# Kernel tuning notes

Measured on AMD Instinct MI355X. Metric: run time of the kernel, lower is better.

## Reference

```python
import jax, jax.numpy as jnp
import numpy as np

EPS = 1e-5


def _layernorm(x, w, b):
    mu = jnp.mean(x, axis=-1, keepdims=True)
    var = jnp.mean(jnp.square(x - mu), axis=-1, keepdims=True)
    return (x - mu) * jax.lax.rsqrt(var + EPS) * w + b


def setup_inputs() -> dict:
    key = jax.random.key(0)
    ks = jax.random.split(key, 8)
    B, N, D = 1, 512, 128
    x = jax.random.normal(ks[0], (B, N, N, D), dtype=jnp.float32)
    mask = jnp.round(jax.random.uniform(ks[1], (B, N, N), dtype=jnp.float32) * 0.6 + 0.4)
    # LayerNorm params (input_norm: ones/zeros; output_norm: ones/zeros)
    ln1_w = jnp.ones((D,), jnp.float32)
    ln1_b = jnp.zeros((D,), jnp.float32)
    ln2_w = jnp.ones((D // 2,), jnp.float32)
    ln2_b = jnp.zeros((D // 2,), jnp.float32)
    # Linear weights stored (in, out). pi: lecun-normal; gi/go: gating init (zeros w, ones b); po: final init (zeros) -> use small randn for a nontrivial baseline.
    sd = 1.0 / np.sqrt(D)
    pi_w = jax.random.normal(ks[2], (D, D), jnp.float32) * sd
    pi_b = jnp.zeros((D,), jnp.float32)
    gi_w = jax.random.normal(ks[3], (D, D), jnp.float32) * sd
    gi_b = jnp.ones((D,), jnp.float32)
    sd2 = 1.0 / np.sqrt(D // 2)
    po_w = jax.random.normal(ks[4], (D // 2, D), jnp.float32) * sd2
    po_b = jnp.zeros((D,), jnp.float32)
    go_w = jax.random.normal(ks[5], (D // 2, D), jnp.float32) * sd2
    go_b = jnp.ones((D,), jnp.float32)
    return {"x": x, "mask": mask, "ln1_w": ln1_w, "ln1_b": ln1_b,
            "pi_w": pi_w, "pi_b": pi_b, "gi_w": gi_w, "gi_b": gi_b,
            "ln2_w": ln2_w, "ln2_b": ln2_b, "po_w": po_w, "po_b": po_b,
            "go_w": go_w, "go_b": go_b}


def reference(x, mask, ln1_w, ln1_b, pi_w, pi_b, gi_w, gi_b,
              ln2_w, ln2_b, po_w, po_b, go_w, go_b):
    # project_and_gate: LN -> pi/gi linears -> sigmoid gate -> mask
    h = _layernorm(x, ln1_w, ln1_b)                      # (B,N,N,D)
    pi_out = h @ pi_w + pi_b
    gi_logits = h @ gi_w + gi_b
    g = pi_out * jax.nn.sigmoid(gi_logits) * mask[..., None]
    # triangular multiplication: split channels into 4 groups of D/4
    a1, b1, a2, b2 = jnp.split(g, 4, axis=-1)            # each (B,N,N,D/4)
    x1 = jnp.einsum('bikd,bjkd->bijd', a1, b1)           # k_dim=2 (outgoing)
    x2 = jnp.einsum('bkid,bkjd->bijd', a2, b2)           # k_dim=1 (incoming)
    t = jnp.concatenate([x1, x2], axis=-1)               # (B,N,N,D/2)
    # output: LN -> po/go linears -> sigmoid gate -> mask
    t = _layernorm(t, ln2_w, ln2_b)
    po_out = t @ po_w + po_b                             # (B,N,N,D)
    go_logits = t @ go_w + go_b
    return po_out * jax.nn.sigmoid(go_logits) * mask[..., None]
```

## Files before the change

kernel.cpp:

```cpp
#include <hip/hip_runtime.h>
#include <hip/hip_bf16.h>

#define NDIM 512
#define NN   (NDIM * NDIM)


using short8 = __attribute__((ext_vector_type(8))) short;
using f32x4  = __attribute__((ext_vector_type(4))) float;
typedef unsigned int uint32;
typedef unsigned short ushort;

__device__ __forceinline__ float sigmoidf_(float z) { return 1.f / (1.f + __expf(-z)); }
__device__ __forceinline__ uint32 pkbf2(float a, float b) {
    __hip_bfloat162 h = __float22bfloat162_rn(float2{a, b});
    uint32 u; __builtin_memcpy(&u, &h, 4); return u;
}
__device__ __forceinline__ ushort bfbits(float f) {
    __hip_bfloat16 h = __float2bfloat16(f);
    ushort u; __builtin_memcpy(&u, &h, 2); return u;
}
__device__ __forceinline__ float bf2f(ushort h) {
    return __uint_as_float(((uint32)h) << 16);
}

__global__ void k_prep(const float* __restrict__ Wp, const float* __restrict__ Wg,
                       const float* __restrict__ lnw, const float* __restrict__ lnb,
                       const float* __restrict__ bp, const float* __restrict__ bg,
                       int K, ushort* __restrict__ dst, float* __restrict__ cb)
{
    __shared__ float red[2][2][128];
    const int nbp = (K * 128) / 256;
    const int tid = threadIdx.x;
    if ((int)blockIdx.x < nbp) {
        const int idx = blockIdx.x * 256 + tid;
        const int k = idx >> 7, o = idx & 127;
        int rowp, rowg;
        if (K == 128) {
            const int h = o >> 6, c = o & 63, q = c >> 5, s = c & 31;
            rowp = h * 128 + q * 64 + s;
            rowg = rowp + 32;
        } else {
            const int q = o >> 6, s = o & 63;
            rowp = q * 128 + s;
            rowg = rowp + 64;
        }
        const float wk = lnw[k];
        const float vp = Wp[k * 128 + o] * wk;
        const float vg = Wg[k * 128 + o] * wk;
        ushort hi;
        hi = bfbits(vp);
        dst[rowp * K + k] = hi;
        dst[256 * K + rowp * K + k] = bfbits(vp - bf2f(hi));
        hi = bfbits(vg);
        dst[rowg * K + k] = hi;
        dst[256 * K + rowg * K + k] = bfbits(vg - bf2f(hi));
    } else {
        const int b = blockIdx.x - nbp;
        const float* W = b ? Wg : Wp;
        const float* bias = b ? bg : bp;
        const int o = tid & 127, kh = tid >> 7;
        const int kham = K >> 1;
        const int k0 = kh * kham;
        float c1 = 0.f, c2 = 0.f;
#pragma unroll 8
        for (int k = 0; k < kham; ++k) {
            const float wv = W[(k0 + k) * 128 + o];
            c1 = fmaf(lnw[k0 + k], wv, c1);
            c2 = fmaf(lnb[k0 + k], wv, c2);
        }
        red[kh][0][o] = c1; red[kh][1][o] = c2;
        __syncthreads();
        if (kh == 0) {
            const int base = b ? 256 : 0;
            cb[base + o] = red[0][0][o] + red[1][0][o];
            cb[base + 128 + o] = red[0][1][o] + red[1][1][o] + bias[o];
        }
    }
}

__global__ __launch_bounds__(256, 4)
void k_stage1(const float* __restrict__ x, const float* __restrict__ mask,
              const ushort* __restrict__ wt1, const float* __restrict__ cb,
              ushort* __restrict__ wsg)
{
    __shared__ char sbuf[32768];
    __shared__ float Ms[128], Mu[128], Rs[128];

    const int tid = threadIdx.x;
    const int g  = blockIdx.x;
    const int y  = (g >> 3) & 1;
    const int bx = (g & 7) | ((g >> 4) << 3);
    const int o0 = y * 64;
    const int w = tid >> 6, l = tid & 63;
    const int mrow = (w & 1) * 64, ncol = (w >> 1) * 64;

    long posBase, outBase; int stride;
    if (y == 0) {
        posBase = ((long)(bx >> 2)) * 512 + (long)(bx & 3) * 128;
        outBase = posBase; stride = 1;
    } else {
        posBase = ((long)(bx >> 9)) * 65536 + (bx & 511);
        outBase = (long)(bx & 511) * 512 + ((bx >> 9) * 128);
        stride = 512;
    }

    short8 bh[2][4], bl[2][4];
#pragma unroll
    for (int n = 0; n < 4; ++n) {
        const int row = y*128 + ncol + n*16 + (l & 15);
        const int idx = row*128 + (l >> 4)*8;
        bh[0][n] = *(const short8*)(wt1 + idx);
        bl[0][n] = *(const short8*)(wt1 + 32768 + idx);
    }

    {
#pragma unroll
        for (int q = 0; q < 16; ++q) {
            const int idx = q*256 + tid;
            const int pos = idx >> 5, fg = idx & 31;
            const float4 v = *(const float4*)(x + (posBase + (long)pos*stride)*128 + fg*4);
            uint2 pk;
            pk.x = pkbf2(v.x, v.y);
            pk.y = pkbf2(v.z, v.w);
            const int col = (fg*8) ^ ((pos & 15) << 4);
            *(uint2*)(sbuf + pos*256 + col) = pk;
        }
        if (tid < 128) Ms[tid] = mask[posBase + (long)tid * stride];
    }
    __syncthreads();

    {
        const int r = tid >> 1, hf = tid & 1;
        float s = 0.f, ss = 0.f;
#pragma unroll
        for (int c = 0; c < 8; ++c) {
            const int col = (hf*128 + c*16) ^ ((r & 15) << 4);
            const short8 hv = *(const short8*)(sbuf + r*256 + col);
#pragma unroll
            for (int e = 0; e < 8; ++e) {
                const float tv = bf2f((ushort)hv[e]);
                s += tv; ss = fmaf(tv, tv, ss);
            }
        }
        s  += __shfl_xor(s, 1);
        ss += __shfl_xor(ss, 1);
        const float mu = s * (1.f/128.f);
        const float var = ss * (1.f/128.f) - mu*mu;
        const float rstd = rsqrtf(var + 1e-5f);
        if (hf == 0) { Mu[r] = mu; Rs[r] = rstd; }
    }

    f32x4 acc[4][4];
#pragma unroll
    for (int m = 0; m < 4; ++m)
#pragma unroll
        for (int n = 0; n < 4; ++n) acc[m][n] = (f32x4){0.f,0.f,0.f,0.f};

#pragma unroll
    for (int step = 0; step < 4; ++step) {
        if (step < 3) {
            const int s1 = step + 1;
#pragma unroll
            for (int n = 0; n < 4; ++n) {
                const int row = y*128 + ncol + n*16 + (l & 15);
                const int idx = row*128 + s1*32 + (l >> 4)*8;
                bh[s1 & 1][n] = *(const short8*)(wt1 + idx);
                bl[s1 & 1][n] = *(const short8*)(wt1 + 32768 + idx);
            }
        }
        short8 ah[4];
#pragma unroll
        for (int m = 0; m < 4; ++m) {
            const int pos = mrow + m*16 + (l & 15);
            const int col = (step*64 + (l >> 4)*16) ^ ((pos & 15) << 4);
            ah[m] = *(const short8*)(sbuf + pos*256 + col);
        }
#pragma unroll
        for (int m = 0; m < 4; ++m) {
#pragma unroll
            for (int n = 0; n < 4; ++n) {
                acc[m][n] = __builtin_amdgcn_mfma_f32_16x16x32_bf16(ah[m], bh[step & 1][n], acc[m][n], 0, 0, 0);
                acc[m][n] = __builtin_amdgcn_mfma_f32_16x16x32_bf16(ah[m], bl[step & 1][n], acc[m][n], 0, 0, 0);
            }
        }
    }
    __syncthreads();

#pragma unroll
    for (int m = 0; m < 4; ++m) {
#pragma unroll
        for (int n = 0; n < 2; ++n) {
            const f32x4 aP = acc[m][n];
            const f32x4 aG = acc[m][n + 2];
            const int cl = (w >> 1)*32 + n*16 + (l & 15);
            const int och = o0 + cl;
            const float c1p = cb[och],       c2p = cb[128 + och];
            const float c1g = cb[256 + och], c2g = cb[384 + och];
            const int p0 = mrow + m*16 + (l >> 4)*4;
            float gv[4];
#pragma unroll
            for (int e = 0; e < 4; ++e) {
                const float mu = Mu[p0+e], rstd = Rs[p0+e];
                const float p_ = fmaf(rstd, aP[e] - mu*c1p, c2p);
                const float g_ = fmaf(rstd, aG[e] - mu*c1g, c2g);
                gv[e] = p_ * sigmoidf_(g_) * Ms[p0+e];
            }
            uint2 pk;
            pk.x = pkbf2(gv[0], gv[1]);
            pk.y = pkbf2(gv[2], gv[3]);
            *(uint2*)(sbuf + cl*256 + ((p0*2) ^ ((cl & 7) << 4))) = pk;
        }
    }
    __syncthreads();

#pragma unroll
    for (int it = 0; it < 2; ++it) {
        const int u = it*256 + tid;
        const int c = u >> 3, seg = u & 7;
        ushort* hd = wsg + (long)(o0 + c) * NN + outBase + seg*16;
#pragma unroll
        for (int q = 0; q < 2; ++q) {
            const short8 v = *(const short8*)(sbuf + c*256 + ((seg*32 + q*16) ^ ((c & 7) << 4)));
            *(short8*)(hd + q*8) = v;
        }
    }
}

__global__ __launch_bounds__(512, 1)
void k_einsum(const ushort* __restrict__ wsg, ushort* __restrict__ wst)
{
    const int bid = blockIdx.x;
    const int nb  = (bid & 7) * 32 + (bid >> 3);
    const int ch  = nb >> 2;
    const int bi  = (nb >> 1) & 1, bj = nb & 1;
    const int pch = (ch < 32) ? ch : ch + 32;

    const ushort* __restrict__ PH = wsg + (long)pch * NN;
    const ushort* __restrict__ QH = wsg + (long)(pch + 32) * NN;
    ushort* __restrict__ T = wst + (long)ch * NN;

    __shared__ char smem[131072];

    const int tid = threadIdx.x;
    const int w = tid >> 6, l = tid & 63;
    const int isB = w >> 2;

    const ushort* sbase = isB ? (QH + (long)bj * 131072) : (PH + (long)bi * 131072);
    int soff[8];
#pragma unroll
    for (int i = 0; i < 8; ++i) {
        const int ci  = ((w & 3) * 8 + i) * 64 + l;
        const int row = ci >> 3, s = ci & 7;
        const int c   = s ^ (row & 7);
        soff[i] = row * 512 + c * 8;
    }
    const int dbase = isB * 32768 + (w & 3) * 8192;

    f32x4 acc[4][8];
#pragma unroll
    for (int m = 0; m < 4; ++m)
#pragma unroll
        for (int n = 0; n < 8; ++n) acc[m][n] = (f32x4){0.f, 0.f, 0.f, 0.f};

    const int wr = w >> 1;
    const int wc = w & 1;

#define STAGE(buf, step)                                                           \
    {                                                                              \
        const int kOff = (step) * 64;                                              \
        _Pragma("unroll")                                                          \
        for (int i = 0; i < 8; ++i) {                                              \
            __builtin_amdgcn_global_load_lds(                                      \
                (const __attribute__((address_space(1))) void*)(sbase + soff[i] + kOff), \
                (__attribute__((address_space(3))) void*)(smem + (buf)*65536 + dbase + i*1024), \
                16, 0, 0);                                                         \
        }                                                                          \
    }

    STAGE(0, 0);
    __syncthreads();

    for (int t = 0; t < 8; ++t) {
        const int cur = t & 1;
        if (t < 7) STAGE(cur ^ 1, t + 1);

        const char* sA = (const char*)smem + cur * 65536;
        const char* sB = sA + 32768;
        const int jc = l >> 4;
        short8 ah[4][2];
#pragma unroll
        for (int m = 0; m < 4; ++m) {
            const int r = wr * 64 + m * 16 + (l & 15);
#pragma unroll
            for (int ks = 0; ks < 2; ++ks)
                ah[m][ks] = *(const short8*)(sA + r * 128 + ((((ks << 2) | jc) ^ (r & 7)) << 4));
        }
#pragma unroll
        for (int n = 0; n < 8; ++n) {
            const int r = wc * 128 + n * 16 + (l & 15);
            short8 bh0 = *(const short8*)(sB + r * 128 + (((0 | jc) ^ (r & 7)) << 4));
            short8 bh1 = *(const short8*)(sB + r * 128 + (((4 | jc) ^ (r & 7)) << 4));
#pragma unroll
            for (int m = 0; m < 4; ++m) {
                acc[m][n] = __builtin_amdgcn_mfma_f32_16x16x32_bf16(ah[m][0], bh0, acc[m][n], 0, 0, 0);
                acc[m][n] = __builtin_amdgcn_mfma_f32_16x16x32_bf16(ah[m][1], bh1, acc[m][n], 0, 0, 0);
            }
        }
        __syncthreads();
    }
#undef STAGE

    const int rbase = bi * 256 + wr * 64;
    const int cbase = bj * 256 + wc * 128;
#pragma unroll
    for (int m = 0; m < 4; ++m) {
#pragma unroll
        for (int n = 0; n < 8; ++n) {
#pragma unroll
            for (int r = 0; r < 4; ++r) {
                const int row = rbase + m * 16 + (l >> 4) * 4 + r;
                const int col = cbase + n * 16 + (l & 15);
                T[(long)row * NDIM + col] = bfbits(acc[m][n][r]);
            }
        }
    }
}

__global__ __launch_bounds__(256, 4)
void k_stage2(const ushort* __restrict__ wst, const float* __restrict__ mask,
              const ushort* __restrict__ wt2, const float* __restrict__ cb,
              float* __restrict__ out)
{
    __shared__ char buf[8192];
    __shared__ float Ms[64], Mu[64], Rs[64];

    const int tid = threadIdx.x;
    const long pos0 = (long)blockIdx.x * 64;
    const int w = tid >> 6, l = tid & 63;
    const int mrow = (w & 1) * 32;
    const int ncol = (w >> 1) * 128;

#pragma unroll
    for (int q = 0; q < 2; ++q) {
        const int u = q*256 + tid, d = u >> 3, p8 = (u & 7) * 8;
        const short8 v = *(const short8*)(wst + (long)d * NN + pos0 + p8);
#pragma unroll
        for (int e = 0; e < 8; ++e) {
            const int row = p8 + e;
            *(ushort*)(buf + row*128 + ((d*2) ^ ((row & 7) << 4))) = v[e];
        }
    }
    if (tid < 64) Ms[tid] = mask[pos0 + tid];
    __syncthreads();

    {
        const int r = tid >> 2, qf = tid & 3;
        float s = 0.f, ss = 0.f;
#pragma unroll
        for (int c = 0; c < 2; ++c) {
            const short8 hv = *(const short8*)(buf + r*128 + ((qf*32 + c*16) ^ ((r & 7) << 4)));
#pragma unroll
            for (int e = 0; e < 8; ++e) {
                const float tv = bf2f((ushort)hv[e]);
                s += tv; ss = fmaf(tv, tv, ss);
            }
        }
        s  += __shfl_xor(s, 1);  s  += __shfl_xor(s, 2);
        ss += __shfl_xor(ss, 1); ss += __shfl_xor(ss, 2);
        const float mu = s * (1.f/64.f);
        const float var = ss * (1.f/64.f) - mu*mu;
        const float rstd = rsqrtf(var + 1e-5f);
        if (qf == 0) { Mu[r] = mu; Rs[r] = rstd; }
    }
    __syncthreads();

    f32x4 acc[2][8];
#pragma unroll
    for (int m = 0; m < 2; ++m)
#pragma unroll
        for (int n = 0; n < 8; ++n) acc[m][n] = (f32x4){0.f,0.f,0.f,0.f};

#pragma unroll
    for (int step = 0; step < 2; ++step) {
        short8 ah[2];
#pragma unroll
        for (int m = 0; m < 2; ++m) {
            const int pos = mrow + m*16 + (l & 15);
            const int col = (step*64 + (l >> 4)*16) ^ ((pos & 7) << 4);
            ah[m] = *(const short8*)(buf + pos*128 + col);
        }
#pragma unroll
        for (int n = 0; n < 8; ++n) {
            const int row = ncol + n*16 + (l & 15);
            const int idx = row*64 + step*32 + (l >> 4)*8;
            const short8 bh = *(const short8*)(wt2 + idx);
            const short8 bl = *(const short8*)(wt2 + 16384 + idx);
#pragma unroll
            for (int m = 0; m < 2; ++m) {
                acc[m][n] = __builtin_amdgcn_mfma_f32_16x16x32_bf16(ah[m], bh, acc[m][n], 0, 0, 0);
                acc[m][n] = __builtin_amdgcn_mfma_f32_16x16x32_bf16(ah[m], bl, acc[m][n], 0, 0, 0);
            }
        }
    }

#pragma unroll
    for (int m = 0; m < 2; ++m) {
#pragma unroll
        for (int n = 0; n < 4; ++n) {
            const f32x4 aP = acc[m][n];
            const f32x4 aG = acc[m][n + 4];
            const int och = (w >> 1)*64 + n*16 + (l & 15);
            const float c1p = cb[och],       c2p = cb[128 + och];
            const float c1g = cb[256 + och], c2g = cb[384 + och];
            const int p0 = mrow + m*16 + (l >> 4)*4;
#pragma unroll
            for (int e = 0; e < 4; ++e) {
                const float mu = Mu[p0+e], rstd = Rs[p0+e];
                const float p_ = fmaf(rstd, aP[e] - mu*c1p, c2p);
                const float g_ = fmaf(rstd, aG[e] - mu*c1g, c2g);
                out[(pos0 + p0 + e)*128 + och] = p_ * sigmoidf_(g_) * Ms[p0+e];
            }
        }
    }
}

extern "C" void kernel_launch(void* const* d_in, const int* in_sizes, int n_in,
                              void* d_out, int out_size, void* d_ws, size_t ws_size,
                              hipStream_t stream)
{
    const float* x     = (const float*)d_in[0];
    const float* mask  = (const float*)d_in[1];
    const float* ln1_w = (const float*)d_in[2];
    const float* ln1_b = (const float*)d_in[3];
    const float* pi_w  = (const float*)d_in[4];
    const float* pi_b  = (const float*)d_in[5];
    const float* gi_w  = (const float*)d_in[6];
    const float* gi_b  = (const float*)d_in[7];
    const float* ln2_w = (const float*)d_in[8];
    const float* ln2_b = (const float*)d_in[9];
    const float* po_w  = (const float*)d_in[10];
    const float* po_b  = (const float*)d_in[11];
    const float* go_w  = (const float*)d_in[12];
    const float* go_b  = (const float*)d_in[13];

    ushort* wsg  = (ushort*)d_ws;
    ushort* wstu = (ushort*)((char*)d_ws + (long)128 * NN * 2);
    ushort* wt1  = wstu;
    float*  cb1  = (float*)(wt1 + 65536);
    ushort* wt2  = (ushort*)((char*)d_ws + (long)192 * NN * 2);
    float*  cb2  = (float*)(wt2 + 32768);

    k_prep<<<66, 256, 0, stream>>>(pi_w, gi_w, ln1_w, ln1_b, pi_b, gi_b, 128, wt1, cb1);
    k_prep<<<34, 256, 0, stream>>>(po_w, go_w, ln2_w, ln2_b, po_b, go_b, 64, wt2, cb2);
    k_stage1<<<4096, 256, 0, stream>>>(x, mask, wt1, cb1, wsg);
    k_einsum<<<256, 512, 0, stream>>>(wsg, wstu);
    k_stage2<<<4096, 256, 0, stream>>>(wstu, mask, wt2, cb2, (float*)d_out);
}
```

Before: 244.9 us.

## Split x staging into halves and overlap second-half conversion with first MFMA steps

After: 289.8 us. +18.3%, slower.

```diff
diff --git a/kernel.cpp b/kernel.cpp
--- a/kernel.cpp
+++ b/kernel.cpp
@@ -113,12 +113,15 @@
         bl[0][n] = *(const short8*)(wt1 + 32768 + idx);
     }
 
+    float4 v1[8];
     {
 #pragma unroll
-        for (int q = 0; q < 16; ++q) {
-            const int idx = q*256 + tid;
-            const int pos = idx >> 5, fg = idx & 31;
-            const float4 v = *(const float4*)(x + (posBase + (long)pos*stride)*128 + fg*4);
+        for (int q = 0; q < 8; ++q) {
+            const int u = q*256 + tid;
+            const int pos = u >> 4, fg = u & 15;
+            const float* xr = x + (posBase + (long)pos*stride)*128;
+            const float4 v = *(const float4*)(xr + fg*4);
+            v1[q] = *(const float4*)(xr + (16 + fg)*4);
             uint2 pk;
             pk.x = pkbf2(v.x, v.y);
             pk.y = pkbf2(v.z, v.w);
@@ -126,6 +129,51 @@
             *(uint2*)(sbuf + pos*256 + col) = pk;
         }
         if (tid < 128) Ms[tid] = mask[posBase + (long)tid * stride];
+    }
+    __syncthreads();
+
+    f32x4 acc[4][4];
+#pragma unroll
+    for (int m = 0; m < 4; ++m)
+#pragma unroll
+        for (int n = 0; n < 4; ++n) acc[m][n] = (f32x4){0.f,0.f,0.f,0.f};
+
+#pragma unroll
+    for (int q = 0; q < 8; ++q) {
+        const int u = q*256 + tid;
+        const int pos = u >> 4, fg = 16 + (u & 15);
+        uint2 pk;
+        pk.x = pkbf2(v1[q].x, v1[q].y);
+        pk.y = pkbf2(v1[q].z, v1[q].w);
+        const int col = (fg*8) ^ ((pos & 15) << 4);
+        *(uint2*)(sbuf + pos*256 + col) = pk;
+    }
+
+#pragma unroll
+    for (int step = 0; step < 2; ++step) {
+        const int s1 = step + 1;
+#pragma unroll
+        for (int n = 0; n < 4; ++n) {
+            const int row = y*128 + ncol + n*16 + (l & 15);
+            const int idx = row*128 + s1*32 + (l >> 4)*8;
+            bh[s1 & 1][n] = *(const short8*)(wt1 + idx);
+            bl[s1 & 1][n] = *(const short8*)(wt1 + 32768 + idx);
+        }
+        short8 ah[4];
+#pragma unroll
+        for (int m = 0; m < 4; ++m) {
+            const int pos = mrow + m*16 + (l & 15);
+            const int col = (step*64 + (l >> 4)*16) ^ ((pos & 15) << 4);
+            ah[m] = *(const short8*)(sbuf + pos*256 + col);
+        }
+#pragma unroll
+        for (int m = 0; m < 4; ++m) {
+#pragma unroll
+            for (int n = 0; n < 4; ++n) {
+                acc[m][n] = __builtin_amdgcn_mfma_f32_16x16x32_bf16(ah[m], bh[step & 1][n], acc[m][n], 0, 0, 0);
+                acc[m][n] = __builtin_amdgcn_mfma_f32_16x16x32_bf16(ah[m], bl[step & 1][n], acc[m][n], 0, 0, 0);
+            }
+        }
     }
     __syncthreads();
 
@@ -150,14 +198,8 @@
         if (hf == 0) { Mu[r] = mu; Rs[r] = rstd; }
     }
 
-    f32x4 acc[4][4];
-#pragma unroll
-    for (int m = 0; m < 4; ++m)
-#pragma unroll
-        for (int n = 0; n < 4; ++n) acc[m][n] = (f32x4){0.f,0.f,0.f,0.f};
-
-#pragma unroll
-    for (int step = 0; step < 4; ++step) {
+#pragma unroll
+    for (int step = 2; step < 4; ++step) {
         if (step < 3) {
             const int s1 = step + 1;
 #pragma unroll
```
